# Kernel tuning notes

Hardware: AMD Instinct MI355X
Metric: run time of the kernel (lower is better)

## Reference

```python
import jax, jax.numpy as jnp
import numpy as np

B, S, D = 4, 2048, 1024
H = 16
HD = D // H

def setup_inputs() -> dict:
    key = jax.random.key(0)
    ks = jax.random.split(key, 5)
    x = jax.random.normal(ks[0], (B, S, D), dtype=jnp.float32)
    # PyTorch Linear: y = x @ W.T + b; store W in torch layout [out, in]
    w_qkv = jax.random.normal(ks[1], (3 * D, D), dtype=jnp.float32) * (1.0 / np.sqrt(D))
    b_qkv = jax.random.normal(ks[2], (3 * D,), dtype=jnp.float32) * 0.01
    w_out = jax.random.normal(ks[3], (D, D), dtype=jnp.float32) * (1.0 / np.sqrt(D))
    b_out = jax.random.normal(ks[4], (D,), dtype=jnp.float32) * 0.01
    return {"x": x, "w_qkv": w_qkv, "b_qkv": b_qkv, "w_out": w_out, "b_out": b_out}

def reference(x, w_qkv, b_qkv, w_out, b_out):
    b, s, d = x.shape
    qkv = x @ w_qkv.T + b_qkv                      # [B,S,3D]
    q, k, v = jnp.split(qkv, 3, axis=2)
    # [B,S,D] -> [B,H,S,HD]
    q = q.reshape(b, s, H, HD).transpose(0, 2, 1, 3)
    k = k.reshape(b, s, H, HD).transpose(0, 2, 1, 3)
    v = v.reshape(b, s, H, HD).transpose(0, 2, 1, 3)
    att = jnp.einsum('bhqd,bhkd->bhqk', q, k) / np.sqrt(HD)
    causal = jnp.tril(jnp.ones((s, s), dtype=bool))
    att = jnp.where(causal[None, None], att, -jnp.inf)
    att = jax.nn.softmax(att, axis=-1)
    y = jnp.einsum('bhqk,bhkd->bhqd', att, v)      # [B,H,S,HD]
    y = y.transpose(0, 2, 1, 3).reshape(b, s, d)
    return y @ w_out.T + b_out
```

## Files before the change

kernel.cpp:

```cpp
#include <hip/hip_runtime.h>
#include <hip/hip_bf16.h>

#define DEV __device__ __forceinline__

typedef __attribute__((ext_vector_type(8))) short bf16x8;
typedef __attribute__((ext_vector_type(4))) float f32x4;

#define BB 4
#define SS 2048
#define DD 1024
#define HH 16
#define HDD 64
#define MM (BB * SS)
#define NQT (SS / 128)

DEV short f2bf(float f) {
  unsigned u = __builtin_bit_cast(unsigned, f);
  u = u + 0x7fffu + ((u >> 16) & 1u);
  return (short)(u >> 16);
}

DEV float fexp2(float x) {
  float r;
  asm("v_exp_f32 %0, %1" : "=v"(r) : "v"(x));
  return r;
}
DEV float frcp(float x) {
  float r;
  asm("v_rcp_f32 %0, %1" : "=v"(r) : "v"(x));
  return r;
}
DEV unsigned cvtpk(float a, float b) {
  unsigned r;
  asm("v_cvt_pk_bf16_f32 %0, %1, %2" : "=v"(r) : "v"(a), "v"(b));
  return r;
}

DEV void gload_lds16(const void* g, void* l) {
  __builtin_amdgcn_global_load_lds((const __attribute__((address_space(1))) void*)g,
                                   (__attribute__((address_space(3))) void*)l, 16, 0, 0);
}

DEV int2 xcd_swizzle() {
  const int nx = gridDim.x;
  const int nwg = nx * gridDim.y;
  const int o = blockIdx.y * nx + blockIdx.x;
  const int wid = (o & 7) * (nwg >> 3) + (o >> 3);
  int2 r; r.x = wid % nx; r.y = wid / nx;
  return r;
}

DEV void cast_range(const float* __restrict__ in, unsigned long long* __restrict__ out,
                    int n4, int start, int stride) {
  for (int i = start; i < n4; i += stride) {
    const float4 f = ((const float4*)in)[i];
    unsigned long long a = (unsigned long long)(unsigned short)f2bf(f.x)
        | ((unsigned long long)(unsigned short)f2bf(f.y) << 16)
        | ((unsigned long long)(unsigned short)f2bf(f.z) << 32)
        | ((unsigned long long)(unsigned short)f2bf(f.w) << 48);
    out[i] = a;
  }
}

__global__ __launch_bounds__(256)
void cast3_f32_bf16(const float* __restrict__ x, unsigned long long* __restrict__ ox, int nx4,
                    const float* __restrict__ wq, unsigned long long* __restrict__ owq, int nwq4,
                    const float* __restrict__ wo, unsigned long long* __restrict__ owo, int nwo4) {
  const int start = blockIdx.x * 256 + threadIdx.x;
  const int stride = gridDim.x * 256;
  cast_range(x, ox, nx4, start, stride);
  cast_range(wq, owq, nwq4, start, stride);
  cast_range(wo, owo, nwo4, start, stride);
}

template<int EPI, int BN, int WGM, int WGN>
__global__ __launch_bounds__(512)
void gemm8(const short* __restrict__ A, const short* __restrict__ Bw,
           const float* __restrict__ bias,
           short* __restrict__ qo, short* __restrict__ ko, short* __restrict__ vo,
           float* __restrict__ co,
           int M, int N, int K) {
  constexpr int WTM = 256 / WGM;
  constexpr int WTN = BN / WGN;
  constexpr int FM = WTM / 16;
  constexpr int FN = WTN / 16;
  constexpr int NBI = BN / 64;
  __shared__ short sA[2][256 * 64];
  __shared__ short sB[2][BN * 64];
  const int tid = threadIdx.x;
  const int lane = tid & 63;
  const int wid = tid >> 6;
  const int wm = wid / WGN, wn = wid % WGN;
  const int2 sw = xcd_swizzle();
  const int m0 = sw.y * 256;
  const int n0 = sw.x * BN;
  const int lr = lane & 15;
  const int lg = lane >> 4;
  const int lm = lr & 7;

  int arow[4], asoff[4], adoff[4];
#pragma unroll
  for (int i = 0; i < 4; ++i) {
    const int e = i * 512 + tid;
    const int row = e >> 3;
    arow[i] = row; asoff[i] = ((e & 7) ^ (row & 7)) * 8; adoff[i] = e * 8;
  }
  int brow[NBI], bsoff[NBI], bdoff[NBI];
#pragma unroll
  for (int i = 0; i < NBI; ++i) {
    const int e = i * 512 + tid;
    const int row = e >> 3;
    brow[i] = row; bsoff[i] = ((e & 7) ^ (row & 7)) * 8; bdoff[i] = e * 8;
  }

  f32x4 acc[FM][FN] = {};
  const int nkt = K >> 6;

#pragma unroll
  for (int i = 0; i < 4; ++i)
    gload_lds16(A + (size_t)(m0 + arow[i]) * K + asoff[i], &sA[0][adoff[i]]);
#pragma unroll
  for (int i = 0; i < NBI; ++i)
    gload_lds16(Bw + (size_t)(n0 + brow[i]) * K + bsoff[i], &sB[0][bdoff[i]]);

  int cur = 0;
  for (int kt = 0; kt < nkt; ++kt) {
    asm volatile("s_waitcnt vmcnt(0)" ::: "memory");
    __builtin_amdgcn_s_barrier();
    if (kt + 1 < nkt) {
      const int k1 = (kt + 1) << 6;
#pragma unroll
      for (int i = 0; i < 4; ++i)
        gload_lds16(A + (size_t)(m0 + arow[i]) * K + k1 + asoff[i], &sA[cur ^ 1][adoff[i]]);
#pragma unroll
      for (int i = 0; i < NBI; ++i)
        gload_lds16(Bw + (size_t)(n0 + brow[i]) * K + k1 + bsoff[i], &sB[cur ^ 1][bdoff[i]]);
    }
    bf16x8 bfr[FN];
#pragma unroll
    for (int q = 0; q < 4; ++q) {
      const int ks = q >> 1, hf = q & 1;
      const int slot = (((ks << 2) + lg) ^ lm) * 8;
      if (hf == 0) {
#pragma unroll
        for (int nf = 0; nf < FN; ++nf)
          bfr[nf] = *(const bf16x8*)&sB[cur][(wn * WTN + nf * 16 + lr) * 64 + slot];
      }
      bf16x8 afr[FM / 2];
#pragma unroll
      for (int f = 0; f < FM / 2; ++f)
        afr[f] = *(const bf16x8*)&sA[cur][(wm * WTM + (hf * (FM / 2) + f) * 16 + lr) * 64 + slot];
      __builtin_amdgcn_s_setprio(1);
#pragma unroll
      for (int f = 0; f < FM / 2; ++f)
#pragma unroll
        for (int nf = 0; nf < FN; ++nf)
          acc[hf * (FM / 2) + f][nf] =
              __builtin_amdgcn_mfma_f32_16x16x32_bf16(afr[f], bfr[nf], acc[hf * (FM / 2) + f][nf], 0, 0, 0);
      __builtin_amdgcn_s_setprio(0);
      if (q < 3) __builtin_amdgcn_s_barrier();
    }
    cur ^= 1;
  }

#pragma unroll
  for (int i = 0; i < FM; ++i) {
#pragma unroll
    for (int j = 0; j < FN; ++j) {
#pragma unroll
      for (int r = 0; r < 4; ++r) {
        const int row = m0 + wm * WTM + i * 16 + lg * 4 + r;
        const int col = n0 + wn * WTN + j * 16 + lr;
        float v = acc[i][j][r] + bias[col];
        if (EPI == 0) {
          const int part = col >> 10, oo = col & 1023;
          const int h = oo >> 6, d = oo & 63;
          const int bb = row >> 11, s = row & 2047;
          if (part == 0)
            qo[(((size_t)bb * HH + h) * SS + s) * HDD + d] = f2bf(v * 0.18033688f);
          else if (part == 1)
            ko[(((size_t)bb * HH + h) * SS + s) * HDD + d] = f2bf(v);
          else {
            const int q2 = (s >> 2) & 15;
            const int tau = (q2 & 8) | ((q2 & 3) << 1) | ((q2 >> 2) & 1);
            vo[(((size_t)bb * HH + h) * HDD + d) * SS + (s & ~63) + (tau << 2) + (s & 3)] = f2bf(v);
          }
        } else {
          co[(size_t)row * N + col] = v;
        }
      }
    }
  }
}

__global__ __launch_bounds__(256)
void attn_fwd(const short* __restrict__ Q, const short* __restrict__ K,
              const short* __restrict__ V, short* __restrict__ Y) {
  __shared__ short sK[2][64 * 64];
  __shared__ short sV[2][64 * 64];
  const int2 sw = xcd_swizzle();
  const int bh = sw.y;
  const int bx = sw.x;
  const int tid = threadIdx.x, lane = tid & 63, w = tid >> 6;
  const size_t bqk = (size_t)bh * (SS * HDD);
  const size_t bv  = (size_t)bh * (HDD * SS);
  const int b = bh >> 4, h = bh & 15;
  const int lr = lane & 15;
  const int lg = lane >> 4;
  const int lm = lr & 7;

  const int e0 = w * 64 + lane;
  const int e1 = 256 + e0;
  const int r0 = e0 >> 3, s0 = ((e0 & 7) ^ (r0 & 7)) * 8;
  const int r1 = e1 >> 3, s1 = ((e1 & 7) ^ (r1 & 7)) * 8;

  for (int qsel = 0; qsel < 2; ++qsel) {
    const int qt = qsel ? (NQT - 1 - bx) : bx;
    const int q0 = qt * 128;
    const int nkv = 2 * qt + 2;

    __syncthreads();

    {
      const short* gK = K + bqk;
      const short* gV = V + bv;
      gload_lds16(gK + (size_t)r0 * HDD + s0, &sK[0][e0 * 8]);
      gload_lds16(gV + (size_t)r0 * SS + s0, &sV[0][e0 * 8]);
      gload_lds16(gK + (size_t)r1 * HDD + s1, &sK[0][e1 * 8]);
      gload_lds16(gV + (size_t)r1 * SS + s1, &sV[0][e1 * 8]);
    }

    const int qbase = q0 + w * 32;
    bf16x8 qf[2][2];
#pragma unroll
    for (int g = 0; g < 2; ++g)
#pragma unroll
      for (int ks = 0; ks < 2; ++ks)
        qf[g][ks] = *(const bf16x8*)&Q[bqk + (size_t)(qbase + g * 16 + lr) * HDD + ks * 32 + lg * 8];

    f32x4 accO[2][4] = {};
    float m_[2] = {-1e30f, -1e30f}, l_[2] = {0.f, 0.f};

    int cur = 0;
    for (int kt = 0; kt < nkv; ++kt) {
      const int kc0 = kt * 64;
      __syncthreads();
      if (kt < nkv - 1) {
        const short* gK = K + bqk + (size_t)(kc0 + 64) * 64;
        const short* gV = V + bv + kc0 + 64;
        gload_lds16(gK + (size_t)r0 * HDD + s0, &sK[cur ^ 1][e0 * 8]);
        gload_lds16(gV + (size_t)r0 * SS + s0, &sV[cur ^ 1][e0 * 8]);
        gload_lds16(gK + (size_t)r1 * HDD + s1, &sK[cur ^ 1][e1 * 8]);
        gload_lds16(gV + (size_t)r1 * SS + s1, &sV[cur ^ 1][e1 * 8]);
      }

      f32x4 st[2][4] = {};
#pragma unroll
      for (int ks = 0; ks < 2; ++ks) {
#pragma unroll
        for (int nf = 0; nf < 4; ++nf) {
          const int row = nf * 16 + lr;
          const bf16x8 kf = *(const bf16x8*)&sK[cur][row * 64 + (((ks << 2) + lg) ^ lm) * 8];
          st[0][nf] = __builtin_amdgcn_mfma_f32_16x16x32_bf16(kf, qf[0][ks], st[0][nf], 0, 0, 0);
          st[1][nf] = __builtin_amdgcn_mfma_f32_16x16x32_bf16(kf, qf[1][ks], st[1][nf], 0, 0, 0);
        }
      }
      if (kt >= nkv - 2) {
#pragma unroll
        for (int g = 0; g < 2; ++g) {
          const int q = qbase + g * 16 + lr;
#pragma unroll
          for (int nf = 0; nf < 4; ++nf)
#pragma unroll
            for (int r = 0; r < 4; ++r) {
              const int k = kc0 + nf * 16 + lg * 4 + r;
              if (k > q) st[g][nf][r] = -1e30f;
            }
        }
      }

      unsigned u[2][4][2];
#pragma unroll
      for (int g = 0; g < 2; ++g) {
        float rm = -1e30f;
#pragma unroll
        for (int r = 0; r < 4; ++r)
          rm = fmaxf(rm, fmaxf(fmaxf(st[g][0][r], st[g][1][r]), fmaxf(st[g][2][r], st[g][3][r])));
        rm = fmaxf(rm, __shfl_xor(rm, 16));
        rm = fmaxf(rm, __shfl_xor(rm, 32));

        const bool need = rm > m_[g] + 11.5416f;
        if (__any(need)) {
          const float mn = fmaxf(m_[g], rm);
          const float scale = fexp2(m_[g] - mn);
          m_[g] = mn;
          l_[g] *= scale;
#pragma unroll
          for (int r = 0; r < 4; ++r) {
            const float scl = __shfl(scale, (lane & 48) + (lg << 2) + r);
#pragma unroll
            for (int df = 0; df < 4; ++df) accO[g][df][r] *= scl;
          }
        }

        float rs = 0.f;
#pragma unroll
        for (int nf = 0; nf < 4; ++nf)
#pragma unroll
          for (int r = 0; r < 4; ++r) {
            const float p = fexp2(st[g][nf][r] - m_[g]);
            st[g][nf][r] = p;
            rs += p;
          }
        rs += __shfl_xor(rs, 16);
        rs += __shfl_xor(rs, 32);
        l_[g] += rs;

#pragma unroll
        for (int nf = 0; nf < 4; ++nf) {
          u[g][nf][0] = cvtpk(st[g][nf][0], st[g][nf][1]);
          u[g][nf][1] = cvtpk(st[g][nf][2], st[g][nf][3]);
        }
      }

#pragma unroll
      for (int c = 0; c < 2; ++c) {
        int4 pw0, pw1;
        pw0.x = (int)u[0][2 * c][0]; pw0.y = (int)u[0][2 * c][1];
        pw0.z = (int)u[0][2 * c + 1][0]; pw0.w = (int)u[0][2 * c + 1][1];
        pw1.x = (int)u[1][2 * c][0]; pw1.y = (int)u[1][2 * c][1];
        pw1.z = (int)u[1][2 * c + 1][0]; pw1.w = (int)u[1][2 * c + 1][1];
        const bf16x8 pf0 = __builtin_bit_cast(bf16x8, pw0);
        const bf16x8 pf1 = __builtin_bit_cast(bf16x8, pw1);
        const int slot = (((c << 2) + lg) ^ lm) * 8;
#pragma unroll
        for (int df = 0; df < 4; ++df) {
          const bf16x8 vf = *(const bf16x8*)&sV[cur][(df * 16 + lr) * 64 + slot];
          accO[0][df] = __builtin_amdgcn_mfma_f32_16x16x32_bf16(pf0, vf, accO[0][df], 0, 0, 0);
          accO[1][df] = __builtin_amdgcn_mfma_f32_16x16x32_bf16(pf1, vf, accO[1][df], 0, 0, 0);
        }
      }
      cur ^= 1;
    }

#pragma unroll
    for (int g = 0; g < 2; ++g)
#pragma unroll
      for (int r = 0; r < 4; ++r) {
        const float lv = __shfl(l_[g], (lane & 48) + (lg << 2) + r);
        const float inv = frcp(lv);
        const int srow2 = qbase + g * 16 + lg * 4 + r;
#pragma unroll
        for (int df = 0; df < 4; ++df) {
          const int dcol = h * HDD + df * 16 + lr;
          Y[((size_t)b * SS + srow2) * DD + dcol] = f2bf(accO[g][df][r] * inv);
        }
      }
  }
}

extern "C" void kernel_launch(void* const* d_in, const int* in_sizes, int n_in,
                              void* d_out, int out_size, void* d_ws, size_t ws_size,
                              hipStream_t stream) {
  const float* x     = (const float*)d_in[0];
  const float* w_qkv = (const float*)d_in[1];
  const float* b_qkv = (const float*)d_in[2];
  const float* w_out = (const float*)d_in[3];
  const float* b_out = (const float*)d_in[4];
  float* out = (float*)d_out;

  const size_t nx = (size_t)MM * DD;
  const size_t nwq = (size_t)3 * DD * DD;
  const size_t nwo = (size_t)DD * DD;

  short* x_bf    = (short*)d_ws;
  short* wqkv_bf = x_bf + nx;
  short* wout_bf = wqkv_bf + nwq;
  short* q_ws    = wout_bf + nwo;
  short* k_ws    = q_ws + nx;
  short* v_ws    = k_ws + nx;
  short* y_ws    = v_ws + nx;

  cast3_f32_bf16<<<dim3(2048), dim3(256), 0, stream>>>(
      x, (unsigned long long*)x_bf, (int)(nx / 4),
      w_qkv, (unsigned long long*)wqkv_bf, (int)(nwq / 4),
      w_out, (unsigned long long*)wout_bf, (int)(nwo / 4));

  gemm8<0, 256, 2, 4><<<dim3(3 * DD / 256, MM / 256), dim3(512), 0, stream>>>(
      x_bf, wqkv_bf, b_qkv, q_ws, k_ws, v_ws, nullptr, MM, 3 * DD, DD);

  attn_fwd<<<dim3(NQT / 2, BB * HH), dim3(256), 0, stream>>>(q_ws, k_ws, v_ws, y_ws);

  gemm8<1, 128, 4, 2><<<dim3(DD / 128, MM / 256), dim3(512), 0, stream>>>(
      y_ws, wout_bf, b_out, nullptr, nullptr, nullptr, out, MM, DD, DD);
}
```

Before: 214.3 us.

## Rework GEMM mainloop into two-stage prefetch pipeline with occupancy two

Replaces the GEMM kernel with a version that prefetches two K-tiles ahead and uses partial vmcnt waits instead of draining all loads each iteration. It loads all A/B fragments for a tile into registers before issuing the next global-to-LDS loads, then runs a single MFMA burst. It also sets launch bounds to two blocks per CU, fixes the warp grid at 2x4, and changes the QKV GEMM N-tile from 256 to 192. The goal is better overlap of memory and MFMA work and more blocks per CU. In exchange it raises register pressure from holding all fragments at once, and a 192-wide tile may use MFMA and LDS less evenly.

```diff
diff --git a/kernel.cpp b/kernel.cpp
--- a/kernel.cpp
+++ b/kernel.cpp
@@ -73,16 +73,15 @@
   cast_range(wo, owo, nwo4, start, stride);
 }
 
-template<int EPI, int BN, int WGM, int WGN>
-__global__ __launch_bounds__(512)
-void gemm8(const short* __restrict__ A, const short* __restrict__ Bw,
-           const float* __restrict__ bias,
-           short* __restrict__ qo, short* __restrict__ ko, short* __restrict__ vo,
-           float* __restrict__ co,
-           int M, int N, int K) {
-  constexpr int WTM = 256 / WGM;
-  constexpr int WTN = BN / WGN;
-  constexpr int FM = WTM / 16;
+template<int EPI, int BN>
+__global__ __launch_bounds__(512, 2)
+void gemm_pipe(const short* __restrict__ A, const short* __restrict__ Bw,
+               const float* __restrict__ bias,
+               short* __restrict__ qo, short* __restrict__ ko, short* __restrict__ vo,
+               float* __restrict__ co,
+               int M, int N, int K) {
+  constexpr int WTN = BN / 4;
+  constexpr int FM = 8;
   constexpr int FN = WTN / 16;
   constexpr int NBI = BN / 64;
   __shared__ short sA[2][256 * 64];
@@ -90,7 +89,7 @@
   const int tid = threadIdx.x;
   const int lane = tid & 63;
   const int wid = tid >> 6;
-  const int wm = wid / WGN, wn = wid % WGN;
+  const int wm = wid >> 2, wn = wid & 3;
   const int2 sw = xcd_swizzle();
   const int m0 = sw.y * 256;
   const int n0 = sw.x * BN;
@@ -122,45 +121,57 @@
 #pragma unroll
   for (int i = 0; i < NBI; ++i)
     gload_lds16(Bw + (size_t)(n0 + brow[i]) * K + bsoff[i], &sB[0][bdoff[i]]);
-
-  int cur = 0;
+#pragma unroll
+  for (int i = 0; i < 4; ++i)
+    gload_lds16(A + (size_t)(m0 + arow[i]) * K + 64 + asoff[i], &sA[1][adoff[i]]);
+#pragma unroll
+  for (int i = 0; i < NBI; ++i)
+    gload_lds16(Bw + (size_t)(n0 + brow[i]) * K + 64 + bsoff[i], &sB[1][bdoff[i]]);
+
   for (int kt = 0; kt < nkt; ++kt) {
-    asm volatile("s_waitcnt vmcnt(0)" ::: "memory");
+    const int cur = kt & 1;
+    if (kt + 1 < nkt) {
+      if constexpr (NBI == 3) asm volatile("s_waitcnt vmcnt(7)" ::: "memory");
+      else                    asm volatile("s_waitcnt vmcnt(6)" ::: "memory");
+    } else {
+      asm volatile("s_waitcnt vmcnt(0)" ::: "memory");
+    }
     __builtin_amdgcn_s_barrier();
-    if (kt + 1 < nkt) {
-      const int k1 = (kt + 1) << 6;
+
+    bf16x8 afr[FM][2], bfr[FN][2];
+#pragma unroll
+    for (int ks = 0; ks < 2; ++ks) {
+      const int slot = (((ks << 2) + lg) ^ lm) * 8;
+#pragma unroll
+      for (int i = 0; i < FM; ++i)
+        afr[i][ks] = *(const bf16x8*)&sA[cur][(wm * 128 + i * 16 + lr) * 64 + slot];
+#pragma unroll
+      for (int j = 0; j < FN; ++j)
+        bfr[j][ks] = *(const bf16x8*)&sB[cur][(wn * WTN + j * 16 + lr) * 64 + slot];
+    }
+    asm volatile("s_waitcnt lgkmcnt(0)" ::: "memory");
+    __builtin_amdgcn_sched_barrier(0);
+    __builtin_amdgcn_s_barrier();
+
+    if (kt + 2 < nkt) {
+      const int k2 = (kt + 2) << 6;
 #pragma unroll
       for (int i = 0; i < 4; ++i)
-        gload_lds16(A + (size_t)(m0 + arow[i]) * K + k1 + asoff[i], &sA[cur ^ 1][adoff[i]]);
+        gload_lds16(A + (size_t)(m0 + arow[i]) * K + k2 + asoff[i], &sA[cur][adoff[i]]);
 #pragma unroll
       for (int i = 0; i < NBI; ++i)
-        gload_lds16(Bw + (size_t)(n0 + brow[i]) * K + k1 + bsoff[i], &sB[cur ^ 1][bdoff[i]]);
-    }
-    bf16x8 bfr[FN];
-#pragma unroll
-    for (int q = 0; q < 4; ++q) {
-      const int ks = q >> 1, hf = q & 1;
-      const int slot = (((ks << 2) + lg) ^ lm) * 8;
-      if (hf == 0) {
-#pragma unroll
-        for (int nf = 0; nf < FN; ++nf)
-          bfr[nf] = *(const bf16x8*)&sB[cur][(wn * WTN + nf * 16 + lr) * 64 + slot];
-      }
-      bf16x8 afr[FM / 2];
-#pragma unroll
-      for (int f = 0; f < FM / 2; ++f)
-        afr[f] = *(const bf16x8*)&sA[cur][(wm * WTM + (hf * (FM / 2) + f) * 16 + lr) * 64 + slot];
-      __builtin_amdgcn_s_setprio(1);
-#pragma unroll
-      for (int f = 0; f < FM / 2; ++f)
-#pragma unroll
-        for (int nf = 0; nf < FN; ++nf)
-          acc[hf * (FM / 2) + f][nf] =
-              __builtin_amdgcn_mfma_f32_16x16x32_bf16(afr[f], bfr[nf], acc[hf * (FM / 2) + f][nf], 0, 0, 0);
-      __builtin_amdgcn_s_setprio(0);
-      if (q < 3) __builtin_amdgcn_s_barrier();
-    }
-    cur ^= 1;
+        gload_lds16(Bw + (size_t)(n0 + brow[i]) * K + k2 + bsoff[i], &sB[cur][bdoff[i]]);
+    }
+
+    __builtin_amdgcn_s_setprio(1);
+#pragma unroll
+    for (int ks = 0; ks < 2; ++ks)
+#pragma unroll
+      for (int i = 0; i < FM; ++i)
+#pragma unroll
+        for (int j = 0; j < FN; ++j)
+          acc[i][j] = __builtin_amdgcn_mfma_f32_16x16x32_bf16(afr[i][ks], bfr[j][ks], acc[i][j], 0, 0, 0);
+    __builtin_amdgcn_s_setprio(0);
   }
 
 #pragma unroll
@@ -169,7 +180,7 @@
     for (int j = 0; j < FN; ++j) {
 #pragma unroll
       for (int r = 0; r < 4; ++r) {
-        const int row = m0 + wm * WTM + i * 16 + lg * 4 + r;
+        const int row = m0 + wm * 128 + i * 16 + lg * 4 + r;
         const int col = n0 + wn * WTN + j * 16 + lr;
         float v = acc[i][j][r] + bias[col];
         if (EPI == 0) {
@@ -386,11 +397,11 @@
       w_qkv, (unsigned long long*)wqkv_bf, (int)(nwq / 4),
       w_out, (unsigned long long*)wout_bf, (int)(nwo / 4));
 
-  gemm8<0, 256, 2, 4><<<dim3(3 * DD / 256, MM / 256), dim3(512), 0, stream>>>(
+  gemm_pipe<0, 192><<<dim3(3 * DD / 192, MM / 256), dim3(512), 0, stream>>>(
       x_bf, wqkv_bf, b_qkv, q_ws, k_ws, v_ws, nullptr, MM, 3 * DD, DD);
 
   attn_fwd<<<dim3(NQT / 2, BB * HH), dim3(256), 0, stream>>>(q_ws, k_ws, v_ws, y_ws);
 
-  gemm8<1, 128, 4, 2><<<dim3(DD / 128, MM / 256), dim3(512), 0, stream>>>(
+  gemm_pipe<1, 128><<<dim3(DD / 128, MM / 256), dim3(512), 0, stream>>>(
       y_ws, wout_bf, b_out, nullptr, nullptr, nullptr, out, MM, DD, DD);
 }
```

After: 195.6 us. 8.7% less time.
